# Kernel optimization log

Measured on AMD Instinct MI355X. Metric: run time of the kernel, lower is better.

Reference implementation:

```python
import jax, jax.numpy as jnp
import numpy as np

TOP_K = 2  # top-k experts per token


def setup_inputs() -> dict:
    key = jax.random.key(0)
    k1, k2, k3, k4, k5 = jax.random.split(key, 5)
    B, S, D = 1, 2048, 2048
    E, F = 8, 1408
    scale = 0.02
    return {
        "hidden_states": jax.random.normal(k1, (B, S, D), dtype=jnp.float32),
        "gate_w": jax.random.normal(k2, (E, D), dtype=jnp.float32) * scale,
        "w_gate": jax.random.normal(k3, (E, D, F), dtype=jnp.float32) * scale,
        "w_up": jax.random.normal(k4, (E, D, F), dtype=jnp.float32) * scale,
        "w_down": jax.random.normal(k5, (E, F, D), dtype=jnp.float32) * scale,
    }


def reference(hidden_states, gate_w, w_gate, w_up, w_down):
    B, S, D = hidden_states.shape
    T = B * S
    x = hidden_states.reshape(T, D)  # flatten tokens, as in forward()

    # Router: combined gate built from per-rank 1-row gates -> [T, E] logits
    router_logits = jnp.einsum("td,ed->te", x, gate_w)
    routing_weights = jax.nn.softmax(router_logits, axis=-1)
    top_w, top_idx = jax.lax.top_k(routing_weights, TOP_K)  # [T, K]

    # Per-token combine weight for each expert (0 if expert not selected).
    # Equivalent to the one_hot expert_mask + index_add combine in the module.
    comb = jnp.zeros((T, gate_w.shape[0]), dtype=routing_weights.dtype)
    comb = comb.at[jnp.arange(T)[:, None], top_idx].add(top_w)  # [T, E]

    # Each expert is a Qwen2 MLP: down(silu(gate(x)) * up(x)).
    # (Dispatch/all-to-all collapses to dense-per-expert + masked combine
    #  on a single device; tokens with comb==0 contribute nothing.)
    g = jnp.einsum("td,edf->etf", x, w_gate)
    u = jnp.einsum("td,edf->etf", x, w_up)
    y = jnp.einsum("etf,efd->etd", jax.nn.silu(g) * u, w_down)  # [E, T, D]

    out = jnp.einsum("te,etd->td", comb, y)  # weighted combine (index_add)
    return out.reshape(B, S, D)
```

## Files before the change

kernel.cpp:

```cpp
#include <hip/hip_runtime.h>
#include <stdint.h>


#define TT 2048
#define DD 2048
#define FF 1408
#define NE 8
#define HROWS 5120
#define TRASH (2*TT)

typedef float f32x4 __attribute__((ext_vector_type(4)));
typedef short bf16x8 __attribute__((ext_vector_type(8)));

__device__ __forceinline__ unsigned short f2bf(float f) {
    unsigned int x = __float_as_uint(f);
    return (unsigned short)((x + 0x7fffu + ((x >> 16) & 1u)) >> 16);
}
__device__ __forceinline__ float bf2f(unsigned short u) {
    union { unsigned int i; float f; } v; v.i = ((unsigned int)u) << 16; return v.f;
}
__device__ __forceinline__ void gld16(const void* g, void* l) {
    __builtin_amdgcn_global_load_lds((const __attribute__((address_space(1))) void*)g,
                                     (__attribute__((address_space(3))) void*)l, 16, 0, 0);
}

__device__ __forceinline__ void treg(const float* __restrict__ src,
                                     unsigned short* __restrict__ dst,
                                     int R, int C, int r0, int c0) {
    const int lane = threadIdx.x & 63, w = threadIdx.x >> 6;
    const int bi = lane >> 3, bj = lane & 7;
    const int sr = r0 + (w & 1) * 64 + bi * 8;
    const int sc = c0 + (w >> 1) * 64 + bj * 8;
    float4 fa[8], fb[8];
#pragma unroll
    for (int k = 0; k < 8; ++k) {
        const float* p = src + (size_t)(sr + k) * C + sc;
        fa[k] = ((const float4*)p)[0];
        fb[k] = ((const float4*)p)[1];
    }
#pragma unroll
    for (int k = 0; k < 8; ++k) {
        uint4 ov; unsigned short* po = (unsigned short*)&ov;
#pragma unroll
        for (int l = 0; l < 8; ++l) {
            float v = (k < 4) ? ((const float*)&fa[l])[k]
                              : ((const float*)&fb[l])[k - 4];
            po[l] = f2bf(v);
        }
        *(uint4*)&dst[(size_t)(sc + k) * R + sr] = ov;
    }
}

__global__ void transpose_gu_kernel(const float* __restrict__ wg,
                                    const float* __restrict__ wu,
                                    unsigned short* __restrict__ WgT,
                                    unsigned short* __restrict__ WuT) {
    const int z = blockIdx.z;
    const float* src; unsigned short* dst;
    if (z < 8) { src = wg + (size_t)z * DD * FF;       dst = WgT + (size_t)z * FF * DD; }
    else       { src = wu + (size_t)(z - 8) * DD * FF; dst = WuT + (size_t)(z - 8) * FF * DD; }
    treg(src, dst, DD, FF, blockIdx.y * 128, blockIdx.x * 128);
}

__global__ void transpose_d_kernel(const float* __restrict__ wd,
                                   unsigned short* __restrict__ WdT) {
    const int z = blockIdx.z;
    treg(wd + (size_t)z * FF * DD, WdT + (size_t)z * DD * FF,
         FF, DD, blockIdx.y * 128, blockIdx.x * 128);
}

__global__ void router_kernel(const float* __restrict__ x,
                              const float* __restrict__ gw,
                              int* __restrict__ cnt,
                              int* __restrict__ tok,
                              float* __restrict__ wtv,
                              int* __restrict__ dstv,
                              unsigned short* __restrict__ xb) {
    const int wv = threadIdx.x >> 6, lane = threadIdx.x & 63;
    const int t = blockIdx.x * 4 + wv;
    float acc[NE];
#pragma unroll
    for (int e = 0; e < NE; ++e) acc[e] = 0.f;
    const float* xr = x + (size_t)t * DD;
    unsigned short* xbr = xb + (size_t)t * DD;
#pragma unroll
    for (int it = 0; it < DD / 256; ++it) {
        const int j = it * 256 + lane * 4;
        float4 xv = *(const float4*)(xr + j);
        short4 o;
        o.x = (short)f2bf(xv.x); o.y = (short)f2bf(xv.y);
        o.z = (short)f2bf(xv.z); o.w = (short)f2bf(xv.w);
        *(short4*)(xbr + j) = o;
#pragma unroll
        for (int e = 0; e < NE; ++e) {
            float4 g = *(const float4*)(gw + e * DD + j);
            acc[e] += xv.x * g.x + xv.y * g.y + xv.z * g.z + xv.w * g.w;
        }
    }
#pragma unroll
    for (int e = 0; e < NE; ++e) {
        float v = acc[e];
        v += __shfl_xor(v, 32); v += __shfl_xor(v, 16); v += __shfl_xor(v, 8);
        v += __shfl_xor(v, 4);  v += __shfl_xor(v, 2);  v += __shfl_xor(v, 1);
        acc[e] = v;
    }
    if (lane == 0) {
        float mx = acc[0];
#pragma unroll
        for (int e = 1; e < NE; ++e) mx = fmaxf(mx, acc[e]);
        float p[NE], s = 0.f;
#pragma unroll
        for (int e = 0; e < NE; ++e) { p[e] = __expf(acc[e] - mx); s += p[e]; }
        int i0 = 0;
#pragma unroll
        for (int e = 1; e < NE; ++e) if (p[e] > p[i0]) i0 = e;
        int i1 = (i0 == 0) ? 1 : 0;
#pragma unroll
        for (int e = 0; e < NE; ++e) if (e != i0 && p[e] > p[i1]) i1 = e;
        float inv = 1.f / s;
        int p0 = atomicAdd(&cnt[i0], 1);
        tok[i0 * TT + p0] = t; wtv[i0 * TT + p0] = p[i0] * inv; dstv[i0 * TT + p0] = 2 * t;
        int p1 = atomicAdd(&cnt[i1], 1);
        tok[i1 * TT + p1] = t; wtv[i1 * TT + p1] = p[i1] * inv; dstv[i1 * TT + p1] = 2 * t + 1;
    }
}

__global__ void finalize_kernel(const int* __restrict__ cnt,
                                int* __restrict__ base,
                                int* __restrict__ cntpad,
                                int* __restrict__ tok,
                                float* __restrict__ wtv,
                                int* __restrict__ dstv) {
    __shared__ int sc[NE], sp[NE];
    if (threadIdx.x == 0) {
        int b = 0;
        for (int e = 0; e < NE; ++e) {
            int c = cnt[e]; int pd = (c + 127) & ~127;
            base[e] = b; cntpad[e] = pd; sc[e] = c; sp[e] = pd; b += pd;
        }
    }
    __syncthreads();
    for (int e = 0; e < NE; ++e)
        for (int i = sc[e] + (int)threadIdx.x; i < sp[e]; i += 256) {
            tok[e * TT + i] = 0; wtv[e * TT + i] = 0.f; dstv[e * TT + i] = TRASH;
        }
}

__launch_bounds__(256, 2)
__global__ void gemm1_kernel(const unsigned short* __restrict__ Xb,
                             const unsigned short* __restrict__ WgT,
                             const unsigned short* __restrict__ WuT,
                             const int* __restrict__ tok,
                             const int* __restrict__ base,
                             const int* __restrict__ cntpad,
                             unsigned short* __restrict__ H) {
    __shared__ unsigned short As[128 * 32];
    __shared__ unsigned short Bg[64 * 32];
    __shared__ unsigned short Bu[64 * 32];
    __shared__ int s_tok[128];

    const int e = blockIdx.z, rb = blockIdx.y, fb = blockIdx.x;
    const int cp = cntpad[e];
    if (rb * 128 >= cp) return;
    const int b0 = base[e];

    const int tid = threadIdx.x;
    if (tid < 128) s_tok[tid] = tok[e * TT + rb * 128 + tid];
    __syncthreads();

    const int w = tid >> 6, lane = tid & 63;
    const int r = lane & 15, q = lane >> 4;
    const int wm = w & 1, wn = w >> 1;

    const int arow = w * 32 + (lane >> 2);
    const int brow = w * 16 + (lane >> 2);
    const int koff = (lane & 3) * 8;
    const unsigned short* ga0 = Xb + (size_t)s_tok[arow] * DD + koff;
    const unsigned short* ga1 = Xb + (size_t)s_tok[arow + 16] * DD + koff;
    const size_t wb = (size_t)e * FF * DD + (size_t)(fb * 64 + brow) * DD + koff;
    const unsigned short* gg = WgT + wb;
    const unsigned short* gu = WuT + wb;
    unsigned short* la0 = As + arow * 32 + koff;
    unsigned short* la1 = la0 + 16 * 32;
    unsigned short* lg  = Bg + brow * 32 + koff;
    unsigned short* lu  = Bu + brow * 32 + koff;

    f32x4 accg[4][2] = {};
    f32x4 accu[4][2] = {};

    for (int kt = 0; kt < DD / 32; ++kt) {
        gld16(ga0, la0); gld16(ga1, la1);
        gld16(gg, lg);   gld16(gu, lu);
        ga0 += 32; ga1 += 32; gg += 32; gu += 32;
        __syncthreads();
        bf16x8 af[4], gf[2], uf[2];
#pragma unroll
        for (int m = 0; m < 4; ++m)
            af[m] = *(const bf16x8*)&As[(wm * 64 + m * 16 + r) * 32 + q * 8];
#pragma unroll
        for (int n = 0; n < 2; ++n) {
            gf[n] = *(const bf16x8*)&Bg[(wn * 32 + n * 16 + r) * 32 + q * 8];
            uf[n] = *(const bf16x8*)&Bu[(wn * 32 + n * 16 + r) * 32 + q * 8];
        }
#pragma unroll
        for (int m = 0; m < 4; ++m)
#pragma unroll
            for (int n = 0; n < 2; ++n) {
                accg[m][n] = __builtin_amdgcn_mfma_f32_16x16x32_bf16(af[m], gf[n], accg[m][n], 0, 0, 0);
                accu[m][n] = __builtin_amdgcn_mfma_f32_16x16x32_bf16(af[m], uf[n], accu[m][n], 0, 0, 0);
            }
        __syncthreads();
    }

    const size_t hr0 = (size_t)(b0 + rb * 128 + wm * 64);
#pragma unroll
    for (int m = 0; m < 4; ++m)
#pragma unroll
        for (int n = 0; n < 2; ++n)
#pragma unroll
            for (int rr = 0; rr < 4; ++rr) {
                float g = accg[m][n][rr], u = accu[m][n][rr];
                float h = (g / (1.f + __expf(-g))) * u;
                int row = m * 16 + q * 4 + rr;
                int col = fb * 64 + wn * 32 + n * 16 + r;
                H[(hr0 + row) * FF + col] = f2bf(h);
            }
}

__launch_bounds__(256, 2)
__global__ void gemm2_kernel(const unsigned short* __restrict__ H,
                             const unsigned short* __restrict__ WdT,
                             const float* __restrict__ wtv,
                             const int* __restrict__ dstv,
                             const int* __restrict__ base,
                             const int* __restrict__ cntpad,
                             unsigned short* __restrict__ Y) {
    __shared__ unsigned short As[128 * 32];
    __shared__ unsigned short Bs[64 * 32];
    __shared__ float s_w[128];
    __shared__ int s_d[128];

    const int e = blockIdx.z, rb = blockIdx.y, db = blockIdx.x;
    const int cp = cntpad[e];
    if (rb * 128 >= cp) return;
    const int b0 = base[e];

    const int tid = threadIdx.x;
    if (tid < 128) {
        int idx = e * TT + rb * 128 + tid;
        s_w[tid] = wtv[idx]; s_d[tid] = dstv[idx];
    }
    __syncthreads();

    const int w = tid >> 6, lane = tid & 63;
    const int r = lane & 15, q = lane >> 4;
    const int wm = w & 1, wn = w >> 1;

    const int arow = w * 32 + (lane >> 2);
    const int brow = w * 16 + (lane >> 2);
    const int koff = (lane & 3) * 8;
    const unsigned short* ga0 = H + (size_t)(b0 + rb * 128 + arow) * FF + koff;
    const unsigned short* ga1 = ga0 + (size_t)16 * FF;
    const unsigned short* gb = WdT + (size_t)e * DD * FF + (size_t)(db * 64 + brow) * FF + koff;
    unsigned short* la0 = As + arow * 32 + koff;
    unsigned short* la1 = la0 + 16 * 32;
    unsigned short* lb  = Bs + brow * 32 + koff;

    f32x4 acc[4][2] = {};

    for (int kt = 0; kt < FF / 32; ++kt) {
        gld16(ga0, la0); gld16(ga1, la1); gld16(gb, lb);
        ga0 += 32; ga1 += 32; gb += 32;
        __syncthreads();
        bf16x8 af[4], bf[2];
#pragma unroll
        for (int m = 0; m < 4; ++m)
            af[m] = *(const bf16x8*)&As[(wm * 64 + m * 16 + r) * 32 + q * 8];
#pragma unroll
        for (int n = 0; n < 2; ++n)
            bf[n] = *(const bf16x8*)&Bs[(wn * 32 + n * 16 + r) * 32 + q * 8];
#pragma unroll
        for (int m = 0; m < 4; ++m)
#pragma unroll
            for (int n = 0; n < 2; ++n)
                acc[m][n] = __builtin_amdgcn_mfma_f32_16x16x32_bf16(af[m], bf[n], acc[m][n], 0, 0, 0);
        __syncthreads();
    }

#pragma unroll
    for (int m = 0; m < 4; ++m)
#pragma unroll
        for (int n = 0; n < 2; ++n)
#pragma unroll
            for (int rr = 0; rr < 4; ++rr) {
                int row = wm * 64 + m * 16 + q * 4 + rr;
                int col = db * 64 + wn * 32 + n * 16 + r;
                float v = s_w[row] * acc[m][n][rr];
                Y[(size_t)s_d[row] * DD + col] = f2bf(v);
            }
}

__global__ void combine_kernel(const unsigned short* __restrict__ Y,
                               float* __restrict__ out) {
    const int t = blockIdx.x;
    const int d = threadIdx.x * 8;
    uint4 a = *(const uint4*)(Y + (size_t)(2 * t) * DD + d);
    uint4 b = *(const uint4*)(Y + (size_t)(2 * t + 1) * DD + d);
    const unsigned short* pa = (const unsigned short*)&a;
    const unsigned short* pb = (const unsigned short*)&b;
    float4 o0, o1;
    o0.x = bf2f(pa[0]) + bf2f(pb[0]);  o0.y = bf2f(pa[1]) + bf2f(pb[1]);
    o0.z = bf2f(pa[2]) + bf2f(pb[2]);  o0.w = bf2f(pa[3]) + bf2f(pb[3]);
    o1.x = bf2f(pa[4]) + bf2f(pb[4]);  o1.y = bf2f(pa[5]) + bf2f(pb[5]);
    o1.z = bf2f(pa[6]) + bf2f(pb[6]);  o1.w = bf2f(pa[7]) + bf2f(pb[7]);
    float* op = out + (size_t)t * DD + d;
    ((float4*)op)[0] = o0;
    ((float4*)op)[1] = o1;
}

extern "C" void kernel_launch(void* const* d_in, const int* in_sizes, int n_in,
                              void* d_out, int out_size, void* d_ws, size_t ws_size,
                              hipStream_t stream) {
    const float* x      = (const float*)d_in[0];
    const float* gw     = (const float*)d_in[1];
    const float* w_gate = (const float*)d_in[2];
    const float* w_up   = (const float*)d_in[3];
    const float* w_down = (const float*)d_in[4];
    float* out = (float*)d_out;

    uint8_t* ws = (uint8_t*)d_ws;
    size_t off = 0;
    auto alloc = [&](size_t bytes) -> void* {
        void* p = ws + off;
        off = (off + bytes + 255) & ~(size_t)255;
        return p;
    };
    int*   cnt    = (int*)  alloc(NE * 4);
    int*   basep  = (int*)  alloc(NE * 4);
    int*   cntpad = (int*)  alloc(NE * 4);
    int*   tok    = (int*)  alloc((size_t)NE * TT * 4);
    float* wtv    = (float*)alloc((size_t)NE * TT * 4);
    int*   dstv   = (int*)  alloc((size_t)NE * TT * 4);
    unsigned short* Xb  = (unsigned short*)alloc((size_t)TT * DD * 2);
    unsigned short* Hb  = (unsigned short*)alloc((size_t)HROWS * FF * 2);
    unsigned short* Yb  = (unsigned short*)alloc((size_t)(2 * TT + 8) * DD * 2);
    unsigned short* WT  = (unsigned short*)alloc((size_t)2 * NE * FF * DD * 2);
    unsigned short* WgT = WT;
    unsigned short* WuT = WT + (size_t)NE * FF * DD;
    unsigned short* WdT = WT;
    (void)ws_size; (void)in_sizes; (void)n_in; (void)out_size;

    hipMemsetAsync(cnt, 0, NE * 4, stream);
    transpose_gu_kernel<<<dim3(11, 16, 16), 256, 0, stream>>>(w_gate, w_up, WgT, WuT);
    router_kernel<<<dim3(TT / 4), 256, 0, stream>>>(x, gw, cnt, tok, wtv, dstv, Xb);
    finalize_kernel<<<1, 256, 0, stream>>>(cnt, basep, cntpad, tok, wtv, dstv);
    gemm1_kernel<<<dim3(FF / 64, TT / 128, NE), 256, 0, stream>>>(Xb, WgT, WuT, tok, basep, cntpad, Hb);
    transpose_d_kernel<<<dim3(16, 11, 8), 256, 0, stream>>>(w_down, WdT);
    gemm2_kernel<<<dim3(DD / 64, TT / 128, NE), 256, 0, stream>>>(Hb, WdT, wtv, dstv, basep, cntpad, Yb);
    combine_kernel<<<dim3(TT), 256, 0, stream>>>(Yb, out);
}
```

Measured before the change: 530.0 us.

## Fuse finalize into router, combine via atomics in gemm2, widen K-step to 64

Merges the finalize step into the router kernel using a last-block-done counter. It also removes the bf16 Y buffer and the combine kernel: gemm2 now atomically adds weighted fp32 results straight into a zeroed output. The GEMM main loops load two 32-wide K slices per barrier, which halves the number of syncs. The cost is an output memset, 2x shared memory, and fp32 atomics to global memory, with nondeterministic summation order.

```diff
diff --git a/kernel.cpp b/kernel.cpp
--- a/kernel.cpp
+++ b/kernel.cpp
@@ -7,7 +7,6 @@
 #define FF 1408
 #define NE 8
 #define HROWS 5120
-#define TRASH (2*TT)
 
 typedef float f32x4 __attribute__((ext_vector_type(4)));
 typedef short bf16x8 __attribute__((ext_vector_type(8)));
@@ -15,9 +14,6 @@
 __device__ __forceinline__ unsigned short f2bf(float f) {
     unsigned int x = __float_as_uint(f);
     return (unsigned short)((x + 0x7fffu + ((x >> 16) & 1u)) >> 16);
-}
-__device__ __forceinline__ float bf2f(unsigned short u) {
-    union { unsigned int i; float f; } v; v.i = ((unsigned int)u) << 16; return v.f;
 }
 __device__ __forceinline__ void gld16(const void* g, void* l) {
     __builtin_amdgcn_global_load_lds((const __attribute__((address_space(1))) void*)g,
@@ -74,8 +70,13 @@
                               int* __restrict__ cnt,
                               int* __restrict__ tok,
                               float* __restrict__ wtv,
-                              int* __restrict__ dstv,
-                              unsigned short* __restrict__ xb) {
+                              int* __restrict__ tdx,
+                              unsigned short* __restrict__ xb,
+                              int* __restrict__ basep,
+                              int* __restrict__ cntpad) {
+    __shared__ int s_last;
+    __shared__ int sc[NE], sp[NE];
+
     const int wv = threadIdx.x >> 6, lane = threadIdx.x & 63;
     const int t = blockIdx.x * 4 + wv;
     float acc[NE];
@@ -119,31 +120,33 @@
         for (int e = 0; e < NE; ++e) if (e != i0 && p[e] > p[i1]) i1 = e;
         float inv = 1.f / s;
         int p0 = atomicAdd(&cnt[i0], 1);
-        tok[i0 * TT + p0] = t; wtv[i0 * TT + p0] = p[i0] * inv; dstv[i0 * TT + p0] = 2 * t;
+        tok[i0 * TT + p0] = t; wtv[i0 * TT + p0] = p[i0] * inv; tdx[i0 * TT + p0] = t;
         int p1 = atomicAdd(&cnt[i1], 1);
-        tok[i1 * TT + p1] = t; wtv[i1 * TT + p1] = p[i1] * inv; dstv[i1 * TT + p1] = 2 * t + 1;
-    }
-}
-
-__global__ void finalize_kernel(const int* __restrict__ cnt,
-                                int* __restrict__ base,
-                                int* __restrict__ cntpad,
-                                int* __restrict__ tok,
-                                float* __restrict__ wtv,
-                                int* __restrict__ dstv) {
-    __shared__ int sc[NE], sp[NE];
+        tok[i1 * TT + p1] = t; wtv[i1 * TT + p1] = p[i1] * inv; tdx[i1 * TT + p1] = t;
+    }
+
+    __syncthreads();
     if (threadIdx.x == 0) {
-        int b = 0;
-        for (int e = 0; e < NE; ++e) {
-            int c = cnt[e]; int pd = (c + 127) & ~127;
-            base[e] = b; cntpad[e] = pd; sc[e] = c; sp[e] = pd; b += pd;
-        }
+        __threadfence();
+        int d = atomicAdd(&cnt[NE], 1);
+        s_last = (d == (TT / 4) - 1) ? 1 : 0;
     }
     __syncthreads();
-    for (int e = 0; e < NE; ++e)
-        for (int i = sc[e] + (int)threadIdx.x; i < sp[e]; i += 256) {
-            tok[e * TT + i] = 0; wtv[e * TT + i] = 0.f; dstv[e * TT + i] = TRASH;
-        }
+    if (s_last) {
+        if (threadIdx.x == 0) {
+            int b = 0;
+            for (int e = 0; e < NE; ++e) {
+                int c = atomicAdd(&cnt[e], 0);
+                int pd = (c + 127) & ~127;
+                basep[e] = b; cntpad[e] = pd; sc[e] = c; sp[e] = pd; b += pd;
+            }
+        }
+        __syncthreads();
+        for (int e = 0; e < NE; ++e)
+            for (int i = sc[e] + (int)threadIdx.x; i < sp[e]; i += 256) {
+                tok[e * TT + i] = 0; wtv[e * TT + i] = 0.f; tdx[e * TT + i] = 0;
+            }
+    }
 }
 
 __launch_bounds__(256, 2)
@@ -154,9 +157,9 @@
                              const int* __restrict__ base,
                              const int* __restrict__ cntpad,
                              unsigned short* __restrict__ H) {
-    __shared__ unsigned short As[128 * 32];
-    __shared__ unsigned short Bg[64 * 32];
-    __shared__ unsigned short Bu[64 * 32];
+    __shared__ unsigned short As[2 * 128 * 32];
+    __shared__ unsigned short Bg[2 * 64 * 32];
+    __shared__ unsigned short Bu[2 * 64 * 32];
     __shared__ int s_tok[128];
 
     const int e = blockIdx.z, rb = blockIdx.y, fb = blockIdx.x;
@@ -188,27 +191,35 @@
     f32x4 accg[4][2] = {};
     f32x4 accu[4][2] = {};
 
-    for (int kt = 0; kt < DD / 32; ++kt) {
-        gld16(ga0, la0); gld16(ga1, la1);
-        gld16(gg, lg);   gld16(gu, lu);
-        ga0 += 32; ga1 += 32; gg += 32; gu += 32;
-        __syncthreads();
-        bf16x8 af[4], gf[2], uf[2];
-#pragma unroll
-        for (int m = 0; m < 4; ++m)
-            af[m] = *(const bf16x8*)&As[(wm * 64 + m * 16 + r) * 32 + q * 8];
-#pragma unroll
-        for (int n = 0; n < 2; ++n) {
-            gf[n] = *(const bf16x8*)&Bg[(wn * 32 + n * 16 + r) * 32 + q * 8];
-            uf[n] = *(const bf16x8*)&Bu[(wn * 32 + n * 16 + r) * 32 + q * 8];
-        }
-#pragma unroll
-        for (int m = 0; m < 4; ++m)
+    for (int kt = 0; kt < DD / 64; ++kt) {
+        gld16(ga0, la0);           gld16(ga1, la1);
+        gld16(gg,  lg);            gld16(gu,  lu);
+        gld16(ga0 + 32, la0 + 4096); gld16(ga1 + 32, la1 + 4096);
+        gld16(gg + 32,  lg + 2048);  gld16(gu + 32,  lu + 2048);
+        ga0 += 64; ga1 += 64; gg += 64; gu += 64;
+        __syncthreads();
+#pragma unroll
+        for (int h = 0; h < 2; ++h) {
+            const unsigned short* Ah = As + h * 4096;
+            const unsigned short* Gh = Bg + h * 2048;
+            const unsigned short* Uh = Bu + h * 2048;
+            bf16x8 af[4], gf[2], uf[2];
+#pragma unroll
+            for (int m = 0; m < 4; ++m)
+                af[m] = *(const bf16x8*)&Ah[(wm * 64 + m * 16 + r) * 32 + q * 8];
 #pragma unroll
             for (int n = 0; n < 2; ++n) {
-                accg[m][n] = __builtin_amdgcn_mfma_f32_16x16x32_bf16(af[m], gf[n], accg[m][n], 0, 0, 0);
-                accu[m][n] = __builtin_amdgcn_mfma_f32_16x16x32_bf16(af[m], uf[n], accu[m][n], 0, 0, 0);
-            }
+                gf[n] = *(const bf16x8*)&Gh[(wn * 32 + n * 16 + r) * 32 + q * 8];
+                uf[n] = *(const bf16x8*)&Uh[(wn * 32 + n * 16 + r) * 32 + q * 8];
+            }
+#pragma unroll
+            for (int m = 0; m < 4; ++m)
+#pragma unroll
+                for (int n = 0; n < 2; ++n) {
+                    accg[m][n] = __builtin_amdgcn_mfma_f32_16x16x32_bf16(af[m], gf[n], accg[m][n], 0, 0, 0);
+                    accu[m][n] = __builtin_amdgcn_mfma_f32_16x16x32_bf16(af[m], uf[n], accu[m][n], 0, 0, 0);
+                }
+        }
         __syncthreads();
     }
 
@@ -231,14 +242,14 @@
 __global__ void gemm2_kernel(const unsigned short* __restrict__ H,
                              const unsigned short* __restrict__ WdT,
                              const float* __restrict__ wtv,
-                             const int* __restrict__ dstv,
+                             const int* __restrict__ tdx,
                              const int* __restrict__ base,
                              const int* __restrict__ cntpad,
-                             unsigned short* __restrict__ Y) {
-    __shared__ unsigned short As[128 * 32];
-    __shared__ unsigned short Bs[64 * 32];
+                             float* __restrict__ out) {
+    __shared__ unsigned short As[2 * 128 * 32];
+    __shared__ unsigned short Bs[2 * 64 * 32];
     __shared__ float s_w[128];
-    __shared__ int s_d[128];
+    __shared__ int s_t[128];
 
     const int e = blockIdx.z, rb = blockIdx.y, db = blockIdx.x;
     const int cp = cntpad[e];
@@ -248,7 +259,7 @@
     const int tid = threadIdx.x;
     if (tid < 128) {
         int idx = e * TT + rb * 128 + tid;
-        s_w[tid] = wtv[idx]; s_d[tid] = dstv[idx];
+        s_w[tid] = wtv[idx]; s_t[tid] = tdx[idx];
     }
     __syncthreads();
 
@@ -268,22 +279,30 @@
 
     f32x4 acc[4][2] = {};
 
-    for (int kt = 0; kt < FF / 32; ++kt) {
-        gld16(ga0, la0); gld16(ga1, la1); gld16(gb, lb);
-        ga0 += 32; ga1 += 32; gb += 32;
-        __syncthreads();
-        bf16x8 af[4], bf[2];
-#pragma unroll
-        for (int m = 0; m < 4; ++m)
-            af[m] = *(const bf16x8*)&As[(wm * 64 + m * 16 + r) * 32 + q * 8];
-#pragma unroll
-        for (int n = 0; n < 2; ++n)
-            bf[n] = *(const bf16x8*)&Bs[(wn * 32 + n * 16 + r) * 32 + q * 8];
-#pragma unroll
-        for (int m = 0; m < 4; ++m)
+    for (int kt = 0; kt < FF / 64; ++kt) {
+        gld16(ga0, la0);           gld16(ga1, la1);
+        gld16(gb,  lb);
+        gld16(ga0 + 32, la0 + 4096); gld16(ga1 + 32, la1 + 4096);
+        gld16(gb + 32,  lb + 2048);
+        ga0 += 64; ga1 += 64; gb += 64;
+        __syncthreads();
+#pragma unroll
+        for (int h = 0; h < 2; ++h) {
+            const unsigned short* Ah = As + h * 4096;
+            const unsigned short* Bh = Bs + h * 2048;
+            bf16x8 af[4], bf[2];
+#pragma unroll
+            for (int m = 0; m < 4; ++m)
+                af[m] = *(const bf16x8*)&Ah[(wm * 64 + m * 16 + r) * 32 + q * 8];
 #pragma unroll
             for (int n = 0; n < 2; ++n)
-                acc[m][n] = __builtin_amdgcn_mfma_f32_16x16x32_bf16(af[m], bf[n], acc[m][n], 0, 0, 0);
+                bf[n] = *(const bf16x8*)&Bh[(wn * 32 + n * 16 + r) * 32 + q * 8];
+#pragma unroll
+            for (int m = 0; m < 4; ++m)
+#pragma unroll
+                for (int n = 0; n < 2; ++n)
+                    acc[m][n] = __builtin_amdgcn_mfma_f32_16x16x32_bf16(af[m], bf[n], acc[m][n], 0, 0, 0);
+        }
         __syncthreads();
     }
 
@@ -295,27 +314,8 @@
             for (int rr = 0; rr < 4; ++rr) {
                 int row = wm * 64 + m * 16 + q * 4 + rr;
                 int col = db * 64 + wn * 32 + n * 16 + r;
-                float v = s_w[row] * acc[m][n][rr];
-                Y[(size_t)s_d[row] * DD + col] = f2bf(v);
-            }
-}
-
-__global__ void combine_kernel(const unsigned short* __restrict__ Y,
-                               float* __restrict__ out) {
-    const int t = blockIdx.x;
-    const int d = threadIdx.x * 8;
-    uint4 a = *(const uint4*)(Y + (size_t)(2 * t) * DD + d);
-    uint4 b = *(const uint4*)(Y + (size_t)(2 * t + 1) * DD + d);
-    const unsigned short* pa = (const unsigned short*)&a;
-    const unsigned short* pb = (const unsigned short*)&b;
-    float4 o0, o1;
-    o0.x = bf2f(pa[0]) + bf2f(pb[0]);  o0.y = bf2f(pa[1]) + bf2f(pb[1]);
-    o0.z = bf2f(pa[2]) + bf2f(pb[2]);  o0.w = bf2f(pa[3]) + bf2f(pb[3]);
-    o1.x = bf2f(pa[4]) + bf2f(pb[4]);  o1.y = bf2f(pa[5]) + bf2f(pb[5]);
-    o1.z = bf2f(pa[6]) + bf2f(pb[6]);  o1.w = bf2f(pa[7]) + bf2f(pb[7]);
-    float* op = out + (size_t)t * DD + d;
-    ((float4*)op)[0] = o0;
-    ((float4*)op)[1] = o1;
+                atomicAdd(out + (size_t)s_t[row] * DD + col, s_w[row] * acc[m][n][rr]);
+            }
 }
 
 extern "C" void kernel_launch(void* const* d_in, const int* in_sizes, int n_in,
@@ -335,27 +335,25 @@
         off = (off + bytes + 255) & ~(size_t)255;
         return p;
     };
-    int*   cnt    = (int*)  alloc(NE * 4);
+    int*   cnt    = (int*)  alloc((NE + 1) * 4);
     int*   basep  = (int*)  alloc(NE * 4);
     int*   cntpad = (int*)  alloc(NE * 4);
     int*   tok    = (int*)  alloc((size_t)NE * TT * 4);
     float* wtv    = (float*)alloc((size_t)NE * TT * 4);
-    int*   dstv   = (int*)  alloc((size_t)NE * TT * 4);
+    int*   tdx    = (int*)  alloc((size_t)NE * TT * 4);
     unsigned short* Xb  = (unsigned short*)alloc((size_t)TT * DD * 2);
     unsigned short* Hb  = (unsigned short*)alloc((size_t)HROWS * FF * 2);
-    unsigned short* Yb  = (unsigned short*)alloc((size_t)(2 * TT + 8) * DD * 2);
     unsigned short* WT  = (unsigned short*)alloc((size_t)2 * NE * FF * DD * 2);
     unsigned short* WgT = WT;
     unsigned short* WuT = WT + (size_t)NE * FF * DD;
     unsigned short* WdT = WT;
     (void)ws_size; (void)in_sizes; (void)n_in; (void)out_size;
 
-    hipMemsetAsync(cnt, 0, NE * 4, stream);
+    hipMemsetAsync(cnt, 0, (NE + 1) * 4, stream);
+    hipMemsetAsync(out, 0, (size_t)TT * DD * 4, stream);
     transpose_gu_kernel<<<dim3(11, 16, 16), 256, 0, stream>>>(w_gate, w_up, WgT, WuT);
-    router_kernel<<<dim3(TT / 4), 256, 0, stream>>>(x, gw, cnt, tok, wtv, dstv, Xb);
-    finalize_kernel<<<1, 256, 0, stream>>>(cnt, basep, cntpad, tok, wtv, dstv);
+    router_kernel<<<dim3(TT / 4), 256, 0, stream>>>(x, gw, cnt, tok, wtv, tdx, Xb, basep, cntpad);
     gemm1_kernel<<<dim3(FF / 64, TT / 128, NE), 256, 0, stream>>>(Xb, WgT, WuT, tok, basep, cntpad, Hb);
     transpose_d_kernel<<<dim3(16, 11, 8), 256, 0, stream>>>(w_down, WdT);
-    gemm2_kernel<<<dim3(DD / 64, TT / 128, NE), 256, 0, stream>>>(Hb, WdT, wtv, dstv, basep, cntpad, Yb);
-    combine_kernel<<<dim3(TT), 256, 0, stream>>>(Yb, out);
-}
+    gemm2_kernel<<<dim3(DD / 64, TT / 128, NE), 256, 0, stream>>>(Hb, WdT, wtv, tdx, basep, cntpad, out);
+}
```

After: 597.7 us. 12.8% more time.

## Widen GEMM N-tiles to 128 and fold finalize into router via last-block atomic

Applied to the files above, without the earlier changes.

Both expert GEMMs move from 128x64 to 128x128 output tiles, with each wave computing a 64x64 sub-tile. This halves the grid and raises MFMA work per LDS fragment load, so each A tile is reused across twice as many columns. The separate finalize launch is removed: the last router block, found through an atomic completion counter, computes the padded expert offsets and fills the padding slots. The costs are much higher accumulator register pressure in gemm1 (32 f32x4 accumulators under launch_bounds 256,2), fewer blocks to spread over the CUs, and a threadfence/atomic in every router block.

```diff
diff --git a/kernel.cpp b/kernel.cpp
--- a/kernel.cpp
+++ b/kernel.cpp
@@ -75,7 +75,12 @@
                               int* __restrict__ tok,
                               float* __restrict__ wtv,
                               int* __restrict__ dstv,
-                              unsigned short* __restrict__ xb) {
+                              unsigned short* __restrict__ xb,
+                              int* __restrict__ basep,
+                              int* __restrict__ cntpad) {
+    __shared__ int s_last;
+    __shared__ int sc[NE], sp[NE];
+
     const int wv = threadIdx.x >> 6, lane = threadIdx.x & 63;
     const int t = blockIdx.x * 4 + wv;
     float acc[NE];
@@ -123,27 +128,29 @@
         int p1 = atomicAdd(&cnt[i1], 1);
         tok[i1 * TT + p1] = t; wtv[i1 * TT + p1] = p[i1] * inv; dstv[i1 * TT + p1] = 2 * t + 1;
     }
-}
-
-__global__ void finalize_kernel(const int* __restrict__ cnt,
-                                int* __restrict__ base,
-                                int* __restrict__ cntpad,
-                                int* __restrict__ tok,
-                                float* __restrict__ wtv,
-                                int* __restrict__ dstv) {
-    __shared__ int sc[NE], sp[NE];
+
+    __syncthreads();
     if (threadIdx.x == 0) {
-        int b = 0;
-        for (int e = 0; e < NE; ++e) {
-            int c = cnt[e]; int pd = (c + 127) & ~127;
-            base[e] = b; cntpad[e] = pd; sc[e] = c; sp[e] = pd; b += pd;
+        __threadfence();
+        int d = atomicAdd(&cnt[NE], 1);
+        s_last = (d == (TT / 4) - 1) ? 1 : 0;
+    }
+    __syncthreads();
+    if (s_last) {
+        if (threadIdx.x == 0) {
+            int b = 0;
+            for (int e = 0; e < NE; ++e) {
+                int c = atomicAdd(&cnt[e], 0);
+                int pd = (c + 127) & ~127;
+                basep[e] = b; cntpad[e] = pd; sc[e] = c; sp[e] = pd; b += pd;
+            }
         }
-    }
-    __syncthreads();
-    for (int e = 0; e < NE; ++e)
-        for (int i = sc[e] + (int)threadIdx.x; i < sp[e]; i += 256) {
-            tok[e * TT + i] = 0; wtv[e * TT + i] = 0.f; dstv[e * TT + i] = TRASH;
-        }
+        __syncthreads();
+        for (int e = 0; e < NE; ++e)
+            for (int i = sc[e] + (int)threadIdx.x; i < sp[e]; i += 256) {
+                tok[e * TT + i] = 0; wtv[e * TT + i] = 0.f; dstv[e * TT + i] = TRASH;
+            }
+    }
 }
 
 __launch_bounds__(256, 2)
@@ -155,8 +162,8 @@
                              const int* __restrict__ cntpad,
                              unsigned short* __restrict__ H) {
     __shared__ unsigned short As[128 * 32];
-    __shared__ unsigned short Bg[64 * 32];
-    __shared__ unsigned short Bu[64 * 32];
+    __shared__ unsigned short Bg[128 * 32];
+    __shared__ unsigned short Bu[128 * 32];
     __shared__ int s_tok[128];
 
     const int e = blockIdx.z, rb = blockIdx.y, fb = blockIdx.x;
@@ -172,40 +179,44 @@
     const int r = lane & 15, q = lane >> 4;
     const int wm = w & 1, wn = w >> 1;
 
-    const int arow = w * 32 + (lane >> 2);
-    const int brow = w * 16 + (lane >> 2);
+    const int srow = w * 32 + (lane >> 2);
     const int koff = (lane & 3) * 8;
-    const unsigned short* ga0 = Xb + (size_t)s_tok[arow] * DD + koff;
-    const unsigned short* ga1 = Xb + (size_t)s_tok[arow + 16] * DD + koff;
-    const size_t wb = (size_t)e * FF * DD + (size_t)(fb * 64 + brow) * DD + koff;
-    const unsigned short* gg = WgT + wb;
-    const unsigned short* gu = WuT + wb;
-    unsigned short* la0 = As + arow * 32 + koff;
-    unsigned short* la1 = la0 + 16 * 32;
-    unsigned short* lg  = Bg + brow * 32 + koff;
-    unsigned short* lu  = Bu + brow * 32 + koff;
-
-    f32x4 accg[4][2] = {};
-    f32x4 accu[4][2] = {};
+    const unsigned short* ga0 = Xb + (size_t)s_tok[srow] * DD + koff;
+    const unsigned short* ga1 = Xb + (size_t)s_tok[srow + 16] * DD + koff;
+    const size_t wb = (size_t)e * FF * DD + (size_t)(fb * 128 + srow) * DD + koff;
+    const unsigned short* gg0 = WgT + wb;
+    const unsigned short* gg1 = WgT + wb + (size_t)16 * DD;
+    const unsigned short* gu0 = WuT + wb;
+    const unsigned short* gu1 = WuT + wb + (size_t)16 * DD;
+    unsigned short* la0 = As + srow * 32 + koff;
+    unsigned short* la1 = la0 + 512;
+    unsigned short* lg0 = Bg + srow * 32 + koff;
+    unsigned short* lg1 = lg0 + 512;
+    unsigned short* lu0 = Bu + srow * 32 + koff;
+    unsigned short* lu1 = lu0 + 512;
+
+    f32x4 accg[4][4] = {};
+    f32x4 accu[4][4] = {};
 
     for (int kt = 0; kt < DD / 32; ++kt) {
         gld16(ga0, la0); gld16(ga1, la1);
-        gld16(gg, lg);   gld16(gu, lu);
-        ga0 += 32; ga1 += 32; gg += 32; gu += 32;
-        __syncthreads();
-        bf16x8 af[4], gf[2], uf[2];
+        gld16(gg0, lg0); gld16(gg1, lg1);
+        gld16(gu0, lu0); gld16(gu1, lu1);
+        ga0 += 32; ga1 += 32; gg0 += 32; gg1 += 32; gu0 += 32; gu1 += 32;
+        __syncthreads();
+        bf16x8 af[4], gf[4], uf[4];
 #pragma unroll
         for (int m = 0; m < 4; ++m)
             af[m] = *(const bf16x8*)&As[(wm * 64 + m * 16 + r) * 32 + q * 8];
 #pragma unroll
-        for (int n = 0; n < 2; ++n) {
-            gf[n] = *(const bf16x8*)&Bg[(wn * 32 + n * 16 + r) * 32 + q * 8];
-            uf[n] = *(const bf16x8*)&Bu[(wn * 32 + n * 16 + r) * 32 + q * 8];
+        for (int n = 0; n < 4; ++n) {
+            gf[n] = *(const bf16x8*)&Bg[(wn * 64 + n * 16 + r) * 32 + q * 8];
+            uf[n] = *(const bf16x8*)&Bu[(wn * 64 + n * 16 + r) * 32 + q * 8];
         }
 #pragma unroll
         for (int m = 0; m < 4; ++m)
 #pragma unroll
-            for (int n = 0; n < 2; ++n) {
+            for (int n = 0; n < 4; ++n) {
                 accg[m][n] = __builtin_amdgcn_mfma_f32_16x16x32_bf16(af[m], gf[n], accg[m][n], 0, 0, 0);
                 accu[m][n] = __builtin_amdgcn_mfma_f32_16x16x32_bf16(af[m], uf[n], accu[m][n], 0, 0, 0);
             }
@@ -216,13 +227,13 @@
 #pragma unroll
     for (int m = 0; m < 4; ++m)
 #pragma unroll
-        for (int n = 0; n < 2; ++n)
+        for (int n = 0; n < 4; ++n)
 #pragma unroll
             for (int rr = 0; rr < 4; ++rr) {
                 float g = accg[m][n][rr], u = accu[m][n][rr];
                 float h = (g / (1.f + __expf(-g))) * u;
                 int row = m * 16 + q * 4 + rr;
-                int col = fb * 64 + wn * 32 + n * 16 + r;
+                int col = fb * 128 + wn * 64 + n * 16 + r;
                 H[(hr0 + row) * FF + col] = f2bf(h);
             }
 }
@@ -236,7 +247,7 @@
                              const int* __restrict__ cntpad,
                              unsigned short* __restrict__ Y) {
     __shared__ unsigned short As[128 * 32];
-    __shared__ unsigned short Bs[64 * 32];
+    __shared__ unsigned short Bs[128 * 32];
     __shared__ float s_w[128];
     __shared__ int s_d[128];
 
@@ -256,33 +267,35 @@
     const int r = lane & 15, q = lane >> 4;
     const int wm = w & 1, wn = w >> 1;
 
-    const int arow = w * 32 + (lane >> 2);
-    const int brow = w * 16 + (lane >> 2);
+    const int srow = w * 32 + (lane >> 2);
     const int koff = (lane & 3) * 8;
-    const unsigned short* ga0 = H + (size_t)(b0 + rb * 128 + arow) * FF + koff;
+    const unsigned short* ga0 = H + (size_t)(b0 + rb * 128 + srow) * FF + koff;
     const unsigned short* ga1 = ga0 + (size_t)16 * FF;
-    const unsigned short* gb = WdT + (size_t)e * DD * FF + (size_t)(db * 64 + brow) * FF + koff;
-    unsigned short* la0 = As + arow * 32 + koff;
-    unsigned short* la1 = la0 + 16 * 32;
-    unsigned short* lb  = Bs + brow * 32 + koff;
-
-    f32x4 acc[4][2] = {};
+    const unsigned short* gb0 = WdT + (size_t)e * DD * FF + (size_t)(db * 128 + srow) * FF + koff;
+    const unsigned short* gb1 = gb0 + (size_t)16 * FF;
+    unsigned short* la0 = As + srow * 32 + koff;
+    unsigned short* la1 = la0 + 512;
+    unsigned short* lb0 = Bs + srow * 32 + koff;
+    unsigned short* lb1 = lb0 + 512;
+
+    f32x4 acc[4][4] = {};
 
     for (int kt = 0; kt < FF / 32; ++kt) {
-        gld16(ga0, la0); gld16(ga1, la1); gld16(gb, lb);
-        ga0 += 32; ga1 += 32; gb += 32;
-        __syncthreads();
-        bf16x8 af[4], bf[2];
+        gld16(ga0, la0); gld16(ga1, la1);
+        gld16(gb0, lb0); gld16(gb1, lb1);
+        ga0 += 32; ga1 += 32; gb0 += 32; gb1 += 32;
+        __syncthreads();
+        bf16x8 af[4], bf[4];
 #pragma unroll
         for (int m = 0; m < 4; ++m)
             af[m] = *(const bf16x8*)&As[(wm * 64 + m * 16 + r) * 32 + q * 8];
 #pragma unroll
-        for (int n = 0; n < 2; ++n)
-            bf[n] = *(const bf16x8*)&Bs[(wn * 32 + n * 16 + r) * 32 + q * 8];
+        for (int n = 0; n < 4; ++n)
+            bf[n] = *(const bf16x8*)&Bs[(wn * 64 + n * 16 + r) * 32 + q * 8];
 #pragma unroll
         for (int m = 0; m < 4; ++m)
 #pragma unroll
-            for (int n = 0; n < 2; ++n)
+            for (int n = 0; n < 4; ++n)
                 acc[m][n] = __builtin_amdgcn_mfma_f32_16x16x32_bf16(af[m], bf[n], acc[m][n], 0, 0, 0);
         __syncthreads();
     }
@@ -290,11 +303,11 @@
 #pragma unroll
     for (int m = 0; m < 4; ++m)
 #pragma unroll
-        for (int n = 0; n < 2; ++n)
+        for (int n = 0; n < 4; ++n)
 #pragma unroll
             for (int rr = 0; rr < 4; ++rr) {
                 int row = wm * 64 + m * 16 + q * 4 + rr;
-                int col = db * 64 + wn * 32 + n * 16 + r;
+                int col = db * 128 + wn * 64 + n * 16 + r;
                 float v = s_w[row] * acc[m][n][rr];
                 Y[(size_t)s_d[row] * DD + col] = f2bf(v);
             }
@@ -335,7 +348,7 @@
         off = (off + bytes + 255) & ~(size_t)255;
         return p;
     };
-    int*   cnt    = (int*)  alloc(NE * 4);
+    int*   cnt    = (int*)  alloc((NE + 1) * 4);
     int*   basep  = (int*)  alloc(NE * 4);
     int*   cntpad = (int*)  alloc(NE * 4);
     int*   tok    = (int*)  alloc((size_t)NE * TT * 4);
@@ -350,12 +363,11 @@
     unsigned short* WdT = WT;
     (void)ws_size; (void)in_sizes; (void)n_in; (void)out_size;
 
-    hipMemsetAsync(cnt, 0, NE * 4, stream);
+    hipMemsetAsync(cnt, 0, (NE + 1) * 4, stream);
     transpose_gu_kernel<<<dim3(11, 16, 16), 256, 0, stream>>>(w_gate, w_up, WgT, WuT);
-    router_kernel<<<dim3(TT / 4), 256, 0, stream>>>(x, gw, cnt, tok, wtv, dstv, Xb);
-    finalize_kernel<<<1, 256, 0, stream>>>(cnt, basep, cntpad, tok, wtv, dstv);
-    gemm1_kernel<<<dim3(FF / 64, TT / 128, NE), 256, 0, stream>>>(Xb, WgT, WuT, tok, basep, cntpad, Hb);
+    router_kernel<<<dim3(TT / 4), 256, 0, stream>>>(x, gw, cnt, tok, wtv, dstv, Xb, basep, cntpad);
+    gemm1_kernel<<<dim3(FF / 128, TT / 128, NE), 256, 0, stream>>>(Xb, WgT, WuT, tok, basep, cntpad, Hb);
     transpose_d_kernel<<<dim3(16, 11, 8), 256, 0, stream>>>(w_down, WdT);
-    gemm2_kernel<<<dim3(DD / 64, TT / 128, NE), 256, 0, stream>>>(Hb, WdT, wtv, dstv, basep, cntpad, Yb);
+    gemm2_kernel<<<dim3(DD / 128, TT / 128, NE), 256, 0, stream>>>(Hb, WdT, wtv, dstv, basep, cntpad, Yb);
     combine_kernel<<<dim3(TT), 256, 0, stream>>>(Yb, out);
 }
```

Result: faster. 509.4 us (-3.9%).
